# Kernel tuning notes

Measured on AMD Instinct MI355X. Metric: run time of the kernel, lower is better.

## Reference

```python
import jax, jax.numpy as jnp
import numpy as np

S_DIM, H_DIM, A_DIM, EMB, MAX_LEN = 1024, 2048, 166, 256, 20
DEC = H_DIM // 2          # decoder_hidden = 1024
VOCAB = A_DIM + 3         # 169; sos=166, eos=167, pad/ignore=168
SOS, IGNORE = A_DIM, A_DIM + 2
B = 8192


def setup_inputs() -> dict:
    key = jax.random.key(0)
    ks = jax.random.split(key, 12)
    sc = lambda fan: 1.0 / np.sqrt(fan)
    emb = jax.random.normal(ks[0], (VOCAB, EMB), jnp.float32)
    emb = emb.at[IGNORE].set(0.0)  # padding_idx=168 row is zero
    return {
        's': jax.random.normal(ks[1], (B, S_DIM), jnp.float32),
        'a_target_seq': jax.random.randint(ks[2], (B, MAX_LEN), 0, VOCAB, jnp.int32),
        'W1': jax.random.normal(ks[3], (S_DIM, H_DIM), jnp.float32) * sc(S_DIM),
        'b1': jnp.zeros((H_DIM,), jnp.float32),
        'W2': jax.random.normal(ks[4], (H_DIM, DEC), jnp.float32) * sc(H_DIM),
        'b2': jnp.zeros((DEC,), jnp.float32),
        'emb': emb,
        'Wih': jax.random.normal(ks[5], (EMB + DEC, 3 * DEC), jnp.float32) * sc(DEC),
        'Whh': jax.random.normal(ks[6], (DEC, 3 * DEC), jnp.float32) * sc(DEC),
        'bih': jnp.zeros((3 * DEC,), jnp.float32),
        'bhh': jnp.zeros((3 * DEC,), jnp.float32),
        'Wp': jax.random.normal(ks[7], (DEC, VOCAB), jnp.float32) * sc(DEC),
        'bp': jnp.zeros((VOCAB,), jnp.float32),
    }


def _gru_step(h, x, Wih, Whh, bih, bhh):
    # torch nn.GRU cell: gates ordered (r, z, n)
    gi = x @ Wih + bih                      # [B, 3H]
    gh = h @ Whh + bhh                      # [B, 3H]
    ir, iz, inn = jnp.split(gi, 3, axis=-1)
    hr, hz, hn = jnp.split(gh, 3, axis=-1)
    r = jax.nn.sigmoid(ir + hr)
    z = jax.nn.sigmoid(iz + hz)
    n = jnp.tanh(inn + r * hn)
    return (1.0 - z) * n + z * h


def reference(s, a_target_seq, W1, b1, W2, b2, emb, Wih, Whh, bih, bhh, Wp, bp):
    b = s.shape[0]
    h_s = jax.nn.relu(s @ W1 + b1) @ W2 + b2      # net(s): [B, DEC]
    h0 = h_s                                      # concatenated at every step
    # teacher forcing: input token at step t is SOS for t=0 else a_target_seq[:, t-1]
    toks = jnp.concatenate([jnp.full((b, 1), SOS, a_target_seq.dtype),
                            a_target_seq[:, :-1]], axis=1)      # [B, T]

    def step(h, tok_t):
        x = jnp.concatenate([emb[tok_t], h0], axis=-1)          # [B, EMB+DEC]
        h_new = _gru_step(h, x, Wih, Whh, bih, bhh)
        logits = h_new @ Wp + bp                                # [B, VOCAB]
        return h_new, logits

    _, logits_seq = jax.lax.scan(step, h_s, toks.T)             # [T, B, V]
    logits = jnp.transpose(logits_seq, (1, 0, 2))               # [B, T, V]

    # CrossEntropyLoss(ignore_index=IGNORE), mean over non-ignored targets
    flat_logits = logits.reshape(-1, VOCAB)
    flat_tgt = a_target_seq.reshape(-1)
    logp = jax.nn.log_softmax(flat_logits, axis=-1)
    nll = -jnp.take_along_axis(logp, flat_tgt[:, None].astype(jnp.int32), axis=-1)[:, 0]
    mask = (flat_tgt != IGNORE).astype(nll.dtype)
    loss_pred = jnp.sum(nll * mask) / jnp.maximum(jnp.sum(mask), 1.0)

    # pred_act_tsr: scatter 1.0 at per-step argmax, then drop last 3 special tokens
    eval_a = jnp.argmax(logits, axis=-1)                        # [B, T]
    pred_act_tsr = jnp.zeros((b, VOCAB), logits.dtype)
    pred_act_tsr = pred_act_tsr.at[jnp.arange(b)[:, None], eval_a].set(1.0)
    return loss_pred, pred_act_tsr[:, :-3]
```

## Files before the change

kernel.cpp:

```cpp
#include <hip/hip_runtime.h>
#include <math.h>

typedef _Float16 f16;
typedef _Float16 half8 __attribute__((ext_vector_type(8)));
typedef _Float16 half4v __attribute__((ext_vector_type(4)));
typedef float f32x4 __attribute__((ext_vector_type(4)));

#define BATCH 8192
#define SDIM  1024
#define HDIM  2048
#define DECD  1024
#define EMBD  256
#define G3    3072
#define VOCAB 169
#define VPAD  176
#define NFRAG 11
#define TLEN  20
#define SOS_TOK 166
#define IGN_TOK 168
#define OUTC  166

#define GLOAD16(gp, lp) __builtin_amdgcn_global_load_lds( \
    (const __attribute__((address_space(1))) unsigned int*)(gp), \
    (__attribute__((address_space(3))) unsigned int*)(lp), 16, 0, 0)

__device__ __forceinline__ void split2(float a, f16& h, f16& l)
{
    float hi = (fabsf(a) >= 6.103515625e-05f) ? (float)(f16)a : 0.0f;
    h = (f16)hi;
    l = (f16)((a - hi) * 2048.0f);
}

__device__ __forceinline__ float join2(f16 h, f16 l)
{
    return (float)h + (float)l * 4.8828125e-4f;
}

__device__ __forceinline__ int swz(int r, int k0)
{
    const int line = r >> 1;
    const int s = (((r & 1) << 2) | (k0 >> 3)) ^ (line & 7);
    return line * 64 + s * 8;
}

template<int MODE>
__global__ __launch_bounds__(256, 2)
void gemm16(const f16* __restrict__ Ah, const f16* __restrict__ Al,
            const f16* __restrict__ Bh, const f16* __restrict__ Bl,
            const float* __restrict__ bias, float* __restrict__ C,
            f16* __restrict__ Ch, f16* __restrict__ Cl,
            int M, int N, int K, int relu)
{
    __shared__ __align__(16) f16 lds[4][4096];

    const int nx = N >> 7;
    const int cpx = gridDim.x >> 3;
    int wg = blockIdx.x;
    wg = (wg & 7) * cpx + (wg >> 3);
    const int m0 = (wg / nx) << 7;
    const int n0 = (wg % nx) << 7;

    const int tid = threadIdx.x;
    const int w = tid >> 6;
    const int lane = tid & 63;
    const int wr = w >> 1, wc = w & 1;

    const int qq = (lane & 7) ^ (lane >> 3);
    const int row_off = ((lane >> 3) << 1) | (qq >> 2);
    const int k_off = (qq & 3) << 3;
    const f16* sb = (w == 0) ? Ah + (size_t)m0 * K
                  : (w == 1) ? Al + (size_t)m0 * K
                  : (w == 2) ? Bh + (size_t)n0 * K
                             : Bl + (size_t)n0 * K;
    sb += (size_t)row_off * K + k_off;
    f16* lb = &lds[w][0];

    int offA[4], offB[4];
    {
        const int fr = lane & 15, k0 = (lane >> 4) << 3;
#pragma unroll
        for (int t = 0; t < 4; ++t) {
            offA[t] = swz(wr * 64 + t * 16 + fr, k0);
            offB[t] = swz(wc * 64 + t * 16 + fr, k0);
        }
    }

    f32x4 acch[4][4], accl[4][4];
#pragma unroll
    for (int i = 0; i < 4; ++i)
#pragma unroll
        for (int j = 0; j < 4; ++j) { acch[i][j] = (f32x4)0.0f; accl[i][j] = (f32x4)0.0f; }

    const int nkt = K >> 5;
    const size_t K16 = (size_t)K * 16;
    for (int kt = 0; kt < nkt; ++kt) {
        const f16* s = sb + kt * 32;
#pragma unroll
        for (int i = 0; i < 8; ++i)
            GLOAD16(s + (size_t)i * K16, lb + i * 512);
        __syncthreads();

        half8 fah[4], fbh[4], fal[4], fbl[4];
#pragma unroll
        for (int t = 0; t < 4; ++t) {
            fah[t] = *(const half8*)&lds[0][offA[t]];
            fal[t] = *(const half8*)&lds[1][offA[t]];
            fbh[t] = *(const half8*)&lds[2][offB[t]];
            fbl[t] = *(const half8*)&lds[3][offB[t]];
        }
#pragma unroll
        for (int i = 0; i < 4; ++i)
#pragma unroll
            for (int j = 0; j < 4; ++j) {
                acch[i][j] = __builtin_amdgcn_mfma_f32_16x16x32_f16(fah[i], fbh[j], acch[i][j], 0, 0, 0);
                accl[i][j] = __builtin_amdgcn_mfma_f32_16x16x32_f16(fal[i], fbh[j], accl[i][j], 0, 0, 0);
                accl[i][j] = __builtin_amdgcn_mfma_f32_16x16x32_f16(fah[i], fbl[j], accl[i][j], 0, 0, 0);
            }
        __syncthreads();
    }

    const float inv2048 = 4.8828125e-4f;
    const int fr = lane & 15;
    const int fq = lane >> 4;
#pragma unroll
    for (int j = 0; j < 4; ++j) {
        const int col = n0 + wc * 64 + j * 16 + fr;
        const float bc = bias[col];
#pragma unroll
        for (int i = 0; i < 4; ++i) {
            const int row0 = m0 + wr * 64 + i * 16 + fq * 4;
            const f32x4 vh = acch[i][j], vl = accl[i][j];
#pragma unroll
            for (int r = 0; r < 4; ++r) {
                float v = vh[r] + vl[r] * inv2048 + bc;
                if (relu) v = fmaxf(v, 0.0f);
                const size_t o = (size_t)(row0 + r) * N + col;
                if constexpr (MODE & 1) C[o] = v;
                if constexpr (MODE & 2) { f16 hh, hl; split2(v, hh, hl); Ch[o] = hh; Cl[o] = hl; }
            }
        }
    }
}

#define STAGE_V2(KT) do {                                                          \
    const int ko_ = (KT) * 32 + k_off;                                             \
    if (w == 0) {                                                                  \
        const f16* sp = hch + (size_t)(m0 + row_off) * DECD + ko_;                 \
        _Pragma("unroll") for (int i_ = 0; i_ < 8; ++i_)                           \
            GLOAD16(sp + (size_t)i_ * (16 * DECD), &lds[i_ * 512]);                \
    } else if (w == 1) {                                                           \
        const f16* sp = hcl + (size_t)(m0 + row_off) * DECD + ko_;                 \
        _Pragma("unroll") for (int i_ = 0; i_ < 8; ++i_)                           \
            GLOAD16(sp + (size_t)i_ * (16 * DECD), &lds[4096 + i_ * 512]);         \
    } else if (w == 2) {                                                           \
        _Pragma("unroll") for (int g_ = 0; g_ < 3; ++g_) {                         \
            const f16* sp = whh + (size_t)(g_ * DECD + n0 + row_off) * DECD + ko_; \
            _Pragma("unroll") for (int i_ = 0; i_ < 2; ++i_)                       \
                GLOAD16(sp + (size_t)i_ * (16 * DECD),                             \
                        &lds[8192 + g_ * 1024 + i_ * 512]);                        \
        }                                                                          \
    } else {                                                                       \
        _Pragma("unroll") for (int g_ = 0; g_ < 3; ++g_) {                         \
            const f16* sp = whl + (size_t)(g_ * DECD + n0 + row_off) * DECD + ko_; \
            _Pragma("unroll") for (int i_ = 0; i_ < 2; ++i_)                       \
                GLOAD16(sp + (size_t)i_ * (16 * DECD),                             \
                        &lds[11264 + g_ * 1024 + i_ * 512]);                       \
        }                                                                          \
    }                                                                              \
} while (0)

__global__ __launch_bounds__(256, 3)
void gru_fused(const f16* __restrict__ hch, const f16* __restrict__ hcl,
               const f16* __restrict__ whh, const f16* __restrict__ whl,
               const float* __restrict__ bhh, const float* __restrict__ gx0,
               const float* __restrict__ tg, const int* __restrict__ tseq,
               int t, f16* __restrict__ hnh, f16* __restrict__ hnl)
{
    __shared__ __align__(16) f16 lds[14336];

    const int chunk = blockIdx.x & 7;
    const int q     = blockIdx.x >> 3;
    const int m0 = (q >> 2) << 7;
    const int n0 = (chunk * 4 + (q & 3)) << 5;

    const int tid = threadIdx.x, w = tid >> 6, lane = tid & 63;
    const int wr = w >> 1, wc = w & 1;

    const int qq = (lane & 7) ^ (lane >> 3);
    const int row_off = ((lane >> 3) << 1) | (qq >> 2);
    const int k_off = (qq & 3) << 3;

    const int fr = lane & 15, kq8 = (lane >> 4) << 3;
    int offA[4];
#pragma unroll
    for (int i = 0; i < 4; ++i) offA[i] = swz(wr * 64 + i * 16 + fr, kq8);
    const int offB = swz(wc * 16 + fr, kq8);

    f32x4 aH[3][4], aL[3][4];
#pragma unroll
    for (int g = 0; g < 3; ++g)
#pragma unroll
        for (int i = 0; i < 4; ++i) { aH[g][i] = (f32x4)0.0f; aL[g][i] = (f32x4)0.0f; }

    for (int kt = 0; kt < DECD / 32; ++kt) {
        STAGE_V2(kt);
        __syncthreads();

        half8 fah[4], fal[4];
#pragma unroll
        for (int i = 0; i < 4; ++i) {
            fah[i] = *(const half8*)&lds[offA[i]];
            fal[i] = *(const half8*)&lds[4096 + offA[i]];
        }
#pragma unroll
        for (int g = 0; g < 3; ++g) {
            const half8 bh = *(const half8*)&lds[8192 + g * 1024 + offB];
            const half8 bl = *(const half8*)&lds[11264 + g * 1024 + offB];
#pragma unroll
            for (int i = 0; i < 4; ++i) {
                aH[g][i] = __builtin_amdgcn_mfma_f32_16x16x32_f16(fah[i], bh, aH[g][i], 0, 0, 0);
                aL[g][i] = __builtin_amdgcn_mfma_f32_16x16x32_f16(fal[i], bh, aL[g][i], 0, 0, 0);
                aL[g][i] = __builtin_amdgcn_mfma_f32_16x16x32_f16(fah[i], bl, aL[g][i], 0, 0, 0);
            }
        }
        __syncthreads();
    }

    const float inv = 4.8828125e-4f;
    const int fq = lane >> 4;
    const int col = n0 + wc * 16 + fr;
    const float br = bhh[col];
    const float bz = bhh[DECD + col];
    const float bn = bhh[2 * DECD + col];
#pragma unroll
    for (int i = 0; i < 4; ++i) {
#pragma unroll
        for (int r = 0; r < 4; ++r) {
            const int row = m0 + wr * 64 + i * 16 + fq * 4 + r;
            const int tok = (t == 0) ? SOS_TOK : tseq[(size_t)row * TLEN + (t - 1)];
            const size_t gb = (size_t)row * G3;
            const size_t tb = (size_t)tok * G3;
            const float ghr = aH[0][i][r] + aL[0][i][r] * inv + br;
            const float ghz = aH[1][i][r] + aL[1][i][r] * inv + bz;
            const float ghn = aH[2][i][r] + aL[2][i][r] * inv + bn;
            const float gir = gx0[gb + col] + tg[tb + col];
            const float giz = gx0[gb + DECD + col] + tg[tb + DECD + col];
            const float gin = gx0[gb + 2 * DECD + col] + tg[tb + 2 * DECD + col];
            const float rr = 1.f / (1.f + expf(-(gir + ghr)));
            const float zz = 1.f / (1.f + expf(-(giz + ghz)));
            const float nn = tanhf(gin + rr * ghn);
            const size_t hidx = (size_t)row * DECD + col;
            const float hp = join2(hch[hidx], hcl[hidx]);
            const float hv = (1.f - zz) * nn + zz * hp;
            f16 a_, b_; split2(hv, a_, b_);
            hnh[hidx] = a_;
            hnl[hidx] = b_;
        }
    }
}

__global__ __launch_bounds__(256)
void transpose_split(const float* __restrict__ Wm, f16* __restrict__ th, f16* __restrict__ tl,
                     int K, int N)
{
    __shared__ float tile[32][33];
    const int n0 = blockIdx.x << 5, k0 = blockIdx.y << 5;
    const int tx = threadIdx.x & 31, ty = threadIdx.x >> 5;
#pragma unroll
    for (int j = 0; j < 32; j += 8)
        tile[ty + j][tx] = Wm[(size_t)(k0 + ty + j) * N + n0 + tx];
    __syncthreads();
#pragma unroll
    for (int j = 0; j < 32; j += 8) {
        const float a = tile[tx][ty + j];
        f16 hh, hl; split2(a, hh, hl);
        const size_t o = (size_t)(n0 + ty + j) * K + k0 + tx;
        th[o] = hh; tl[o] = hl;
    }
}

__global__ __launch_bounds__(256)
void wp_split(const float* __restrict__ Wp, f16* __restrict__ wph, f16* __restrict__ wpl)
{
    const int k = blockIdx.x * 256 + threadIdx.x;
    const int n = blockIdx.y;
    const float a = (n < VOCAB) ? Wp[(size_t)k * VOCAB + n] : 0.0f;
    f16 h, l; split2(a, h, l);
    wph[(size_t)n * DECD + k] = h;
    wpl[(size_t)n * DECD + k] = l;
}

__global__ __launch_bounds__(256)
void split_act(const float* __restrict__ x, f16* __restrict__ xh, f16* __restrict__ xl)
{
    const int i = blockIdx.x * 256 + threadIdx.x;
    const float4 v = ((const float4*)x)[i];
    half4v hh, hl;
#pragma unroll
    for (int c = 0; c < 4; ++c) { f16 a, b; split2((&v.x)[c], a, b); hh[c] = a; hl[c] = b; }
    ((half4v*)xh)[i] = hh;
    ((half4v*)xl)[i] = hl;
}

__global__ __launch_bounds__(256)
void tok_gi(const float* __restrict__ emb, const float* __restrict__ Wih,
            float* __restrict__ tg)
{
    __shared__ float es[EMBD];
    const int v = blockIdx.y;
    const int n = blockIdx.x * 256 + threadIdx.x;
    es[threadIdx.x] = emb[(size_t)v * EMBD + threadIdx.x];
    __syncthreads();
    float s = 0.f;
#pragma unroll 8
    for (int k = 0; k < EMBD; ++k)
        s = fmaf(es[k], Wih[(size_t)k * G3 + n], s);
    tg[(size_t)v * G3 + n] = s;
}

__global__ __launch_bounds__(256)
void logits_mfma(const f16* __restrict__ hh, const f16* __restrict__ hl,
                 const f16* __restrict__ wph, const f16* __restrict__ wpl,
                 const float* __restrict__ bp, const int* __restrict__ tseq,
                 int t, float* __restrict__ pred, float* __restrict__ accb)
{
    __shared__ float red[3][64][44];
    const int tid = threadIdx.x, wv = tid >> 6, lane = tid & 63;
    const int b0 = blockIdx.x << 4;
    const int fr = lane & 15, kq = lane >> 4;
    const int kb = wv << 8;

    const f16* pa_h = hh + (size_t)(b0 + fr) * DECD + kb + kq * 8;
    const f16* pa_l = hl + (size_t)(b0 + fr) * DECD + kb + kq * 8;
    const f16* pb_h = wph + (size_t)fr * DECD + kb + kq * 8;
    const f16* pb_l = wpl + (size_t)fr * DECD + kb + kq * 8;

    f32x4 acch[NFRAG], accl[NFRAG];
#pragma unroll
    for (int f = 0; f < NFRAG; ++f) { acch[f] = (f32x4)0.0f; accl[f] = (f32x4)0.0f; }

#pragma unroll 2
    for (int kt = 0; kt < 8; ++kt) {
        const int ko = kt * 32;
        const half8 a_h = *(const half8*)(pa_h + ko);
        const half8 a_l = *(const half8*)(pa_l + ko);
#pragma unroll
        for (int f = 0; f < NFRAG; ++f) {
            const half8 b_h = *(const half8*)(pb_h + (size_t)f * 16 * DECD + ko);
            const half8 b_l = *(const half8*)(pb_l + (size_t)f * 16 * DECD + ko);
            acch[f] = __builtin_amdgcn_mfma_f32_16x16x32_f16(a_h, b_h, acch[f], 0, 0, 0);
            accl[f] = __builtin_amdgcn_mfma_f32_16x16x32_f16(a_l, b_h, accl[f], 0, 0, 0);
            accl[f] = __builtin_amdgcn_mfma_f32_16x16x32_f16(a_h, b_l, accl[f], 0, 0, 0);
        }
    }

    float v[44];
#pragma unroll
    for (int f = 0; f < NFRAG; ++f)
#pragma unroll
        for (int r = 0; r < 4; ++r)
            v[f * 4 + r] = acch[f][r] + accl[f][r] * 4.8828125e-4f;

    if (wv > 0) {
#pragma unroll
        for (int idx = 0; idx < 44; ++idx) red[wv - 1][lane][idx] = v[idx];
    }
    __syncthreads();
    if (wv != 0) return;

#pragma unroll
    for (int ww = 0; ww < 3; ++ww)
#pragma unroll
        for (int idx = 0; idx < 44; ++idx) v[idx] += red[ww][lane][idx];

    float wnll = 0.f, wcnt = 0.f;
#pragma unroll
    for (int r = 0; r < 4; ++r) {
        const int b = b0 + kq * 4 + r;
        float vv[NFRAG];
        float m = -3.0e38f; int mi = 0;
#pragma unroll
        for (int f = 0; f < NFRAG; ++f) {
            const int col = f * 16 + fr;
            const float bb = (col < VOCAB) ? bp[col] : -1.0e30f;
            vv[f] = v[f * 4 + r] + bb;
            if (vv[f] > m) { m = vv[f]; mi = col; }
        }
#pragma unroll
        for (int off = 8; off >= 1; off >>= 1) {
            const float om = __shfl_xor(m, off);
            const int   oi = __shfl_xor(mi, off);
            if (om > m || (om == m && oi < mi)) { m = om; mi = oi; }
        }
        const int tgt = tseq[(size_t)b * TLEN + t];
        float se = 0.f, tl = 0.f;
#pragma unroll
        for (int f = 0; f < NFRAG; ++f) {
            se += expf(vv[f] - m);
            if ((tgt >> 4) == f && (tgt & 15) == fr) tl = vv[f];
        }
#pragma unroll
        for (int off = 8; off >= 1; off >>= 1) {
            se += __shfl_xor(se, off);
            tl += __shfl_xor(tl, off);
        }
        if (fr == 0) {
            if (mi < OUTC) pred[(size_t)b * OUTC + mi] = 1.0f;
            if (tgt != IGN_TOK) { wnll += m + logf(se) - tl; wcnt += 1.f; }
        }
    }
    wnll += __shfl_xor(wnll, 16); wnll += __shfl_xor(wnll, 32);
    wcnt += __shfl_xor(wcnt, 16); wcnt += __shfl_xor(wcnt, 32);
    if (lane == 0) {
        atomicAdd(&accb[0], wnll);
        atomicAdd(&accb[1], wcnt);
    }
}

__global__ void finalize_loss(const float* __restrict__ accb, float* __restrict__ out)
{
    out[0] = accb[0] / fmaxf(accb[1], 1.f);
}

extern "C" void kernel_launch(void* const* d_in, const int* in_sizes, int n_in,
                              void* d_out, int out_size, void* d_ws, size_t ws_size,
                              hipStream_t stream)
{
    const float* s    = (const float*)d_in[0];
    const int*   aseq = (const int*)  d_in[1];
    const float* W1   = (const float*)d_in[2];
    const float* b1   = (const float*)d_in[3];
    const float* W2   = (const float*)d_in[4];
    const float* b2   = (const float*)d_in[5];
    const float* emb  = (const float*)d_in[6];
    const float* Wih  = (const float*)d_in[7];
    const float* Whh  = (const float*)d_in[8];
    const float* bih  = (const float*)d_in[9];
    const float* bhh  = (const float*)d_in[10];
    const float* Wp   = (const float*)d_in[11];
    const float* bp   = (const float*)d_in[12];
    float* outp = (float*)d_out;
    char* W = (char*)d_ws;

    const size_t SZ_H = (size_t)BATCH * DECD * 2;
    const size_t o_gx0 = 0;
    const size_t o_hAh = o_gx0 + (size_t)BATCH * G3 * 4;
    const size_t o_hAl = o_hAh + SZ_H;
    const size_t o_hBh = o_hAl + SZ_H;
    const size_t o_hBl = o_hBh + SZ_H;
    const size_t o_tg  = o_hBl + SZ_H;
    const size_t o_whh = o_tg  + (size_t)VOCAB * G3 * 4;
    const size_t o_whl = o_whh + (size_t)DECD * G3 * 2;
    const size_t o_wph = o_whl + (size_t)DECD * G3 * 2;
    const size_t o_wpl = o_wph + (size_t)VPAD * DECD * 2;
    const size_t o_acc = o_wpl + (size_t)VPAD * DECD * 2;
    const size_t need  = o_acc + 256;
    if (ws_size < need) return;

    float* gx0  = (float*)(W + o_gx0);
    f16*   hAh  = (f16*)(W + o_hAh);
    f16*   hAl  = (f16*)(W + o_hAl);
    f16*   hBh  = (f16*)(W + o_hBh);
    f16*   hBl  = (f16*)(W + o_hBl);
    float* tg   = (float*)(W + o_tg);
    f16*   whh  = (f16*)(W + o_whh);
    f16*   whl  = (f16*)(W + o_whl);
    f16*   wph  = (f16*)(W + o_wph);
    f16*   wpl  = (f16*)(W + o_wpl);
    float* accb = (float*)(W + o_acc);

    f16* h1h = (f16*)(W + o_gx0);
    f16* h1l = (f16*)(W + o_gx0 + (size_t)BATCH * HDIM * 2);
    f16* w1h = (f16*)(W + o_gx0 + (size_t)BATCH * HDIM * 4);
    f16* w1l = (f16*)(W + o_gx0 + (size_t)BATCH * HDIM * 4 + (size_t)SDIM * HDIM * 2);
    f16* w2h = w1h;
    f16* w2l = (f16*)(W + o_gx0 + (size_t)BATCH * HDIM * 4 + (size_t)HDIM * DECD * 2);
    f16* sh  = (f16*)(W + o_hBh);
    f16* sl  = (f16*)(W + o_hBh + (size_t)BATCH * SDIM * 2);
    f16* wih = whh;
    f16* wil = whl;

    hipMemsetAsync(d_out, 0, (size_t)out_size * sizeof(float), stream);
    hipMemsetAsync(accb, 0, 2 * sizeof(float), stream);

    split_act<<<dim3(BATCH * SDIM / 4 / 256), 256, 0, stream>>>(s, sh, sl);
    transpose_split<<<dim3(HDIM/32, SDIM/32), 256, 0, stream>>>(W1, w1h, w1l, SDIM, HDIM);
    tok_gi<<<dim3(G3/256, VOCAB), 256, 0, stream>>>(emb, Wih, tg);
    wp_split<<<dim3(DECD/256, VPAD), 256, 0, stream>>>(Wp, wph, wpl);

    gemm16<2><<<dim3((BATCH/128)*(HDIM/128)), 256, 0, stream>>>(
        sh, sl, w1h, w1l, b1, nullptr, h1h, h1l, BATCH, HDIM, SDIM, 1);

    transpose_split<<<dim3(DECD/32, HDIM/32), 256, 0, stream>>>(W2, w2h, w2l, HDIM, DECD);
    gemm16<2><<<dim3((BATCH/128)*(DECD/128)), 256, 0, stream>>>(
        h1h, h1l, w2h, w2l, b2, nullptr, hAh, hAl, BATCH, DECD, HDIM, 0);

    transpose_split<<<dim3(G3/32, DECD/32), 256, 0, stream>>>(Wih + (size_t)EMBD * G3, wih, wil, DECD, G3);
    gemm16<1><<<dim3((BATCH/128)*(G3/128)), 256, 0, stream>>>(
        hAh, hAl, wih, wil, bih, gx0, nullptr, nullptr, BATCH, G3, DECD, 0);

    transpose_split<<<dim3(G3/32, DECD/32), 256, 0, stream>>>(Whh, whh, whl, DECD, G3);

    f16 *ch = hAh, *cl = hAl, *nh = hBh, *nl = hBl;
    for (int t = 0; t < TLEN; ++t) {
        gru_fused<<<dim3((BATCH/128)*(DECD/32)), 256, 0, stream>>>(
            ch, cl, whh, whl, bhh, gx0, tg, aseq, t, nh, nl);
        logits_mfma<<<dim3(BATCH/16), 256, 0, stream>>>(
            nh, nl, wph, wpl, bp, aseq, t, outp + 1, accb);
        f16* tmp;
        tmp = ch; ch = nh; nh = tmp;
        tmp = cl; cl = nl; nl = tmp;
    }
    finalize_loss<<<1, 1, 0, stream>>>(accb, outp);
}
```

Measured before the change: 5.722 ms.

## Fuse GRU step and previous-step logits into one launch with block specialization

Merges the per-step GRU kernel and the logits/loss kernel into a single launch. Extra blocks compute logits for the previous step's hidden state while the GRU blocks compute the next step, so the two phases overlap and the number of launches drops. The logits work is split by vocab fragments across waves instead of by K, with a small LDS reduction, and Wp padding grows to 192 columns. In exchange the launch carries heterogeneous blocks that share one register and launch-bounds budget, and an extra launch is needed after the loop to finish the final step's logits.

Measured after the change: 5.762 ms. About the same (+0.7%).

```diff
diff --git a/kernel.cpp b/kernel.cpp
--- a/kernel.cpp
+++ b/kernel.cpp
@@ -13,12 +13,14 @@
 #define EMBD  256
 #define G3    3072
 #define VOCAB 169
-#define VPAD  176
+#define VPADX 192
 #define NFRAG 11
 #define TLEN  20
 #define SOS_TOK 166
 #define IGN_TOK 168
 #define OUTC  166
+#define NGRU_BLK 2048
+#define NLOG_BLK 512
 
 #define GLOAD16(gp, lp) __builtin_amdgcn_global_load_lds( \
     (const __attribute__((address_space(1))) unsigned int*)(gp), \
@@ -170,91 +172,203 @@
 } while (0)
 
 __global__ __launch_bounds__(256, 3)
-void gru_fused(const f16* __restrict__ hch, const f16* __restrict__ hcl,
-               const f16* __restrict__ whh, const f16* __restrict__ whl,
-               const float* __restrict__ bhh, const float* __restrict__ gx0,
-               const float* __restrict__ tg, const int* __restrict__ tseq,
-               int t, f16* __restrict__ hnh, f16* __restrict__ hnl)
+void step_fused(const f16* __restrict__ hch, const f16* __restrict__ hcl,
+                const f16* __restrict__ whh, const f16* __restrict__ whl,
+                const float* __restrict__ bhh, const float* __restrict__ gx0,
+                const float* __restrict__ tg, const int* __restrict__ tseq,
+                int t, f16* __restrict__ hnh, f16* __restrict__ hnl,
+                const f16* __restrict__ wph, const f16* __restrict__ wpl,
+                const float* __restrict__ bp, int tlog,
+                float* __restrict__ pred, float* __restrict__ accb,
+                int ngru)
 {
     __shared__ __align__(16) f16 lds[14336];
 
-    const int chunk = blockIdx.x & 7;
-    const int q     = blockIdx.x >> 3;
-    const int m0 = (q >> 2) << 7;
-    const int n0 = (chunk * 4 + (q & 3)) << 5;
-
-    const int tid = threadIdx.x, w = tid >> 6, lane = tid & 63;
-    const int wr = w >> 1, wc = w & 1;
-
-    const int qq = (lane & 7) ^ (lane >> 3);
-    const int row_off = ((lane >> 3) << 1) | (qq >> 2);
-    const int k_off = (qq & 3) << 3;
-
-    const int fr = lane & 15, kq8 = (lane >> 4) << 3;
-    int offA[4];
-#pragma unroll
-    for (int i = 0; i < 4; ++i) offA[i] = swz(wr * 64 + i * 16 + fr, kq8);
-    const int offB = swz(wc * 16 + fr, kq8);
-
-    f32x4 aH[3][4], aL[3][4];
-#pragma unroll
-    for (int g = 0; g < 3; ++g)
-#pragma unroll
-        for (int i = 0; i < 4; ++i) { aH[g][i] = (f32x4)0.0f; aL[g][i] = (f32x4)0.0f; }
-
-    for (int kt = 0; kt < DECD / 32; ++kt) {
-        STAGE_V2(kt);
+    if ((int)blockIdx.x < ngru) {
+        const int chunk = blockIdx.x & 7;
+        const int q     = blockIdx.x >> 3;
+        const int m0 = (q >> 2) << 7;
+        const int n0 = (chunk * 4 + (q & 3)) << 5;
+
+        const int tid = threadIdx.x, w = tid >> 6, lane = tid & 63;
+        const int wr = w >> 1, wc = w & 1;
+
+        const int qq = (lane & 7) ^ (lane >> 3);
+        const int row_off = ((lane >> 3) << 1) | (qq >> 2);
+        const int k_off = (qq & 3) << 3;
+
+        const int fr = lane & 15, kq8 = (lane >> 4) << 3;
+        int offA[4];
+#pragma unroll
+        for (int i = 0; i < 4; ++i) offA[i] = swz(wr * 64 + i * 16 + fr, kq8);
+        const int offB = swz(wc * 16 + fr, kq8);
+
+        f32x4 aH[3][4], aL[3][4];
+#pragma unroll
+        for (int g = 0; g < 3; ++g)
+#pragma unroll
+            for (int i = 0; i < 4; ++i) { aH[g][i] = (f32x4)0.0f; aL[g][i] = (f32x4)0.0f; }
+
+        for (int kt = 0; kt < DECD / 32; ++kt) {
+            STAGE_V2(kt);
+            __syncthreads();
+
+            half8 fah[4], fal[4];
+#pragma unroll
+            for (int i = 0; i < 4; ++i) {
+                fah[i] = *(const half8*)&lds[offA[i]];
+                fal[i] = *(const half8*)&lds[4096 + offA[i]];
+            }
+#pragma unroll
+            for (int g = 0; g < 3; ++g) {
+                const half8 bh = *(const half8*)&lds[8192 + g * 1024 + offB];
+                const half8 bl = *(const half8*)&lds[11264 + g * 1024 + offB];
+#pragma unroll
+                for (int i = 0; i < 4; ++i) {
+                    aH[g][i] = __builtin_amdgcn_mfma_f32_16x16x32_f16(fah[i], bh, aH[g][i], 0, 0, 0);
+                    aL[g][i] = __builtin_amdgcn_mfma_f32_16x16x32_f16(fal[i], bh, aL[g][i], 0, 0, 0);
+                    aL[g][i] = __builtin_amdgcn_mfma_f32_16x16x32_f16(fah[i], bl, aL[g][i], 0, 0, 0);
+                }
+            }
+            __syncthreads();
+        }
+
+        const float inv = 4.8828125e-4f;
+        const int fq = lane >> 4;
+        const int col = n0 + wc * 16 + fr;
+        const float br = bhh[col];
+        const float bz = bhh[DECD + col];
+        const float bn = bhh[2 * DECD + col];
+#pragma unroll
+        for (int i = 0; i < 4; ++i) {
+#pragma unroll
+            for (int r = 0; r < 4; ++r) {
+                const int row = m0 + wr * 64 + i * 16 + fq * 4 + r;
+                const int tok = (t == 0) ? SOS_TOK : tseq[(size_t)row * TLEN + (t - 1)];
+                const size_t gb = (size_t)row * G3;
+                const size_t tb = (size_t)tok * G3;
+                const float ghr = aH[0][i][r] + aL[0][i][r] * inv + br;
+                const float ghz = aH[1][i][r] + aL[1][i][r] * inv + bz;
+                const float ghn = aH[2][i][r] + aL[2][i][r] * inv + bn;
+                const float gir = gx0[gb + col] + tg[tb + col];
+                const float giz = gx0[gb + DECD + col] + tg[tb + DECD + col];
+                const float gin = gx0[gb + 2 * DECD + col] + tg[tb + 2 * DECD + col];
+                const float rr = 1.f / (1.f + expf(-(gir + ghr)));
+                const float zz = 1.f / (1.f + expf(-(giz + ghz)));
+                const float nn = tanhf(gin + rr * ghn);
+                const size_t hidx = (size_t)row * DECD + col;
+                const float hp = join2(hch[hidx], hcl[hidx]);
+                const float hv = (1.f - zz) * nn + zz * hp;
+                f16 a_, b_; split2(hv, a_, b_);
+                hnh[hidx] = a_;
+                hnl[hidx] = b_;
+            }
+        }
+    } else {
+        float* red = (float*)&lds[0];
+        const int tid = threadIdx.x, wv = tid >> 6, lane = tid & 63;
+        const int lb = blockIdx.x - ngru;
+        const int b0 = lb << 4;
+        const int fr = lane & 15, kq = lane >> 4;
+        const int fb0 = wv * 3;
+
+        const f16* pa_h = hch + (size_t)(b0 + fr) * DECD + kq * 8;
+        const f16* pa_l = hcl + (size_t)(b0 + fr) * DECD + kq * 8;
+        const f16* pb_h = wph + (size_t)(fb0 * 16 + fr) * DECD + kq * 8;
+        const f16* pb_l = wpl + (size_t)(fb0 * 16 + fr) * DECD + kq * 8;
+
+        f32x4 acch[3], accl[3];
+#pragma unroll
+        for (int f = 0; f < 3; ++f) { acch[f] = (f32x4)0.0f; accl[f] = (f32x4)0.0f; }
+
+#pragma unroll 2
+        for (int kt = 0; kt < 32; ++kt) {
+            const int ko = kt * 32;
+            const half8 a_h = *(const half8*)(pa_h + ko);
+            const half8 a_l = *(const half8*)(pa_l + ko);
+#pragma unroll
+            for (int f = 0; f < 3; ++f) {
+                const half8 b_h = *(const half8*)(pb_h + (size_t)f * 16 * DECD + ko);
+                const half8 b_l = *(const half8*)(pb_l + (size_t)f * 16 * DECD + ko);
+                acch[f] = __builtin_amdgcn_mfma_f32_16x16x32_f16(a_h, b_h, acch[f], 0, 0, 0);
+                accl[f] = __builtin_amdgcn_mfma_f32_16x16x32_f16(a_l, b_h, accl[f], 0, 0, 0);
+                accl[f] = __builtin_amdgcn_mfma_f32_16x16x32_f16(a_h, b_l, accl[f], 0, 0, 0);
+            }
+        }
+
+        const float inv = 4.8828125e-4f;
+#pragma unroll
+        for (int r = 0; r < 4; ++r) {
+            float vv[3];
+            float m = -3.0e38f; int mi = 0;
+#pragma unroll
+            for (int f = 0; f < 3; ++f) {
+                const int col = (fb0 + f) * 16 + fr;
+                const float bb = (col < VOCAB) ? bp[col] : -1.0e30f;
+                vv[f] = acch[f][r] + accl[f][r] * inv + bb;
+                if (vv[f] > m) { m = vv[f]; mi = col; }
+            }
+#pragma unroll
+            for (int off = 8; off >= 1; off >>= 1) {
+                const float om = __shfl_xor(m, off);
+                const int   oi = __shfl_xor(mi, off);
+                if (om > m || (om == m && oi < mi)) { m = om; mi = oi; }
+            }
+            const int b = b0 + kq * 4 + r;
+            const int tgt = tseq[(size_t)b * TLEN + tlog];
+            float se = 0.f, tl = 0.f;
+#pragma unroll
+            for (int f = 0; f < 3; ++f) {
+                se += expf(vv[f] - m);
+                const int col = (fb0 + f) * 16 + fr;
+                if (col == tgt) tl = vv[f];
+            }
+#pragma unroll
+            for (int off = 8; off >= 1; off >>= 1) {
+                se += __shfl_xor(se, off);
+                tl += __shfl_xor(tl, off);
+            }
+            if (fr == 0) {
+                const int row = kq * 4 + r;
+                red[(wv * 16 + row) * 4 + 0] = m;
+                red[(wv * 16 + row) * 4 + 1] = (float)mi;
+                red[(wv * 16 + row) * 4 + 2] = se;
+                red[(wv * 16 + row) * 4 + 3] = tl;
+            }
+        }
         __syncthreads();
 
-        half8 fah[4], fal[4];
-#pragma unroll
-        for (int i = 0; i < 4; ++i) {
-            fah[i] = *(const half8*)&lds[offA[i]];
-            fal[i] = *(const half8*)&lds[4096 + offA[i]];
-        }
-#pragma unroll
-        for (int g = 0; g < 3; ++g) {
-            const half8 bh = *(const half8*)&lds[8192 + g * 1024 + offB];
-            const half8 bl = *(const half8*)&lds[11264 + g * 1024 + offB];
-#pragma unroll
-            for (int i = 0; i < 4; ++i) {
-                aH[g][i] = __builtin_amdgcn_mfma_f32_16x16x32_f16(fah[i], bh, aH[g][i], 0, 0, 0);
-                aL[g][i] = __builtin_amdgcn_mfma_f32_16x16x32_f16(fal[i], bh, aL[g][i], 0, 0, 0);
-                aL[g][i] = __builtin_amdgcn_mfma_f32_16x16x32_f16(fah[i], bl, aL[g][i], 0, 0, 0);
-            }
-        }
-        __syncthreads();
-    }
-
-    const float inv = 4.8828125e-4f;
-    const int fq = lane >> 4;
-    const int col = n0 + wc * 16 + fr;
-    const float br = bhh[col];
-    const float bz = bhh[DECD + col];
-    const float bn = bhh[2 * DECD + col];
-#pragma unroll
-    for (int i = 0; i < 4; ++i) {
-#pragma unroll
-        for (int r = 0; r < 4; ++r) {
-            const int row = m0 + wr * 64 + i * 16 + fq * 4 + r;
-            const int tok = (t == 0) ? SOS_TOK : tseq[(size_t)row * TLEN + (t - 1)];
-            const size_t gb = (size_t)row * G3;
-            const size_t tb = (size_t)tok * G3;
-            const float ghr = aH[0][i][r] + aL[0][i][r] * inv + br;
-            const float ghz = aH[1][i][r] + aL[1][i][r] * inv + bz;
-            const float ghn = aH[2][i][r] + aL[2][i][r] * inv + bn;
-            const float gir = gx0[gb + col] + tg[tb + col];
-            const float giz = gx0[gb + DECD + col] + tg[tb + DECD + col];
-            const float gin = gx0[gb + 2 * DECD + col] + tg[tb + 2 * DECD + col];
-            const float rr = 1.f / (1.f + expf(-(gir + ghr)));
-            const float zz = 1.f / (1.f + expf(-(giz + ghz)));
-            const float nn = tanhf(gin + rr * ghn);
-            const size_t hidx = (size_t)row * DECD + col;
-            const float hp = join2(hch[hidx], hcl[hidx]);
-            const float hv = (1.f - zz) * nn + zz * hp;
-            f16 a_, b_; split2(hv, a_, b_);
-            hnh[hidx] = a_;
-            hnl[hidx] = b_;
+        float wnll = 0.f, wcnt = 0.f;
+        if (wv == 0 && lane < 16) {
+            const int row = lane;
+            float M = red[row * 4 + 0];
+            int  MI = (int)red[row * 4 + 1];
+#pragma unroll
+            for (int wq = 1; wq < 4; ++wq) {
+                const float mw = red[(wq * 16 + row) * 4 + 0];
+                if (mw > M) { M = mw; MI = (int)red[(wq * 16 + row) * 4 + 1]; }
+            }
+            float se = 0.f, tl = 0.f;
+#pragma unroll
+            for (int wq = 0; wq < 4; ++wq) {
+                se += red[(wq * 16 + row) * 4 + 2] * expf(red[(wq * 16 + row) * 4 + 0] - M);
+                tl += red[(wq * 16 + row) * 4 + 3];
+            }
+            const int b = b0 + row;
+            if (MI < OUTC) pred[(size_t)b * OUTC + MI] = 1.0f;
+            const int tgt = tseq[(size_t)b * TLEN + tlog];
+            if (tgt != IGN_TOK) { wnll = M + logf(se) - tl; wcnt = 1.f; }
+        }
+        if (wv == 0) {
+#pragma unroll
+            for (int off = 32; off >= 1; off >>= 1) {
+                wnll += __shfl_xor(wnll, off);
+                wcnt += __shfl_xor(wcnt, off);
+            }
+            if (lane == 0) {
+                atomicAdd(&accb[0], wnll);
+                atomicAdd(&accb[1], wcnt);
+            }
         }
     }
 }
@@ -316,105 +430,6 @@
     for (int k = 0; k < EMBD; ++k)
         s = fmaf(es[k], Wih[(size_t)k * G3 + n], s);
     tg[(size_t)v * G3 + n] = s;
-}
-
-__global__ __launch_bounds__(256)
-void logits_mfma(const f16* __restrict__ hh, const f16* __restrict__ hl,
-                 const f16* __restrict__ wph, const f16* __restrict__ wpl,
-                 const float* __restrict__ bp, const int* __restrict__ tseq,
-                 int t, float* __restrict__ pred, float* __restrict__ accb)
-{
-    __shared__ float red[3][64][44];
-    const int tid = threadIdx.x, wv = tid >> 6, lane = tid & 63;
-    const int b0 = blockIdx.x << 4;
-    const int fr = lane & 15, kq = lane >> 4;
-    const int kb = wv << 8;
-
-    const f16* pa_h = hh + (size_t)(b0 + fr) * DECD + kb + kq * 8;
-    const f16* pa_l = hl + (size_t)(b0 + fr) * DECD + kb + kq * 8;
-    const f16* pb_h = wph + (size_t)fr * DECD + kb + kq * 8;
-    const f16* pb_l = wpl + (size_t)fr * DECD + kb + kq * 8;
-
-    f32x4 acch[NFRAG], accl[NFRAG];
-#pragma unroll
-    for (int f = 0; f < NFRAG; ++f) { acch[f] = (f32x4)0.0f; accl[f] = (f32x4)0.0f; }
-
-#pragma unroll 2
-    for (int kt = 0; kt < 8; ++kt) {
-        const int ko = kt * 32;
-        const half8 a_h = *(const half8*)(pa_h + ko);
-        const half8 a_l = *(const half8*)(pa_l + ko);
-#pragma unroll
-        for (int f = 0; f < NFRAG; ++f) {
-            const half8 b_h = *(const half8*)(pb_h + (size_t)f * 16 * DECD + ko);
-            const half8 b_l = *(const half8*)(pb_l + (size_t)f * 16 * DECD + ko);
-            acch[f] = __builtin_amdgcn_mfma_f32_16x16x32_f16(a_h, b_h, acch[f], 0, 0, 0);
-            accl[f] = __builtin_amdgcn_mfma_f32_16x16x32_f16(a_l, b_h, accl[f], 0, 0, 0);
-            accl[f] = __builtin_amdgcn_mfma_f32_16x16x32_f16(a_h, b_l, accl[f], 0, 0, 0);
-        }
-    }
-
-    float v[44];
-#pragma unroll
-    for (int f = 0; f < NFRAG; ++f)
-#pragma unroll
-        for (int r = 0; r < 4; ++r)
-            v[f * 4 + r] = acch[f][r] + accl[f][r] * 4.8828125e-4f;
-
-    if (wv > 0) {
-#pragma unroll
-        for (int idx = 0; idx < 44; ++idx) red[wv - 1][lane][idx] = v[idx];
-    }
-    __syncthreads();
-    if (wv != 0) return;
-
-#pragma unroll
-    for (int ww = 0; ww < 3; ++ww)
-#pragma unroll
-        for (int idx = 0; idx < 44; ++idx) v[idx] += red[ww][lane][idx];
-
-    float wnll = 0.f, wcnt = 0.f;
-#pragma unroll
-    for (int r = 0; r < 4; ++r) {
-        const int b = b0 + kq * 4 + r;
-        float vv[NFRAG];
-        float m = -3.0e38f; int mi = 0;
-#pragma unroll
-        for (int f = 0; f < NFRAG; ++f) {
-            const int col = f * 16 + fr;
-            const float bb = (col < VOCAB) ? bp[col] : -1.0e30f;
-            vv[f] = v[f * 4 + r] + bb;
-            if (vv[f] > m) { m = vv[f]; mi = col; }
-        }
-#pragma unroll
-        for (int off = 8; off >= 1; off >>= 1) {
-            const float om = __shfl_xor(m, off);
-            const int   oi = __shfl_xor(mi, off);
-            if (om > m || (om == m && oi < mi)) { m = om; mi = oi; }
-        }
-        const int tgt = tseq[(size_t)b * TLEN + t];
-        float se = 0.f, tl = 0.f;
-#pragma unroll
-        for (int f = 0; f < NFRAG; ++f) {
-            se += expf(vv[f] - m);
-            if ((tgt >> 4) == f && (tgt & 15) == fr) tl = vv[f];
-        }
-#pragma unroll
-        for (int off = 8; off >= 1; off >>= 1) {
-            se += __shfl_xor(se, off);
-            tl += __shfl_xor(tl, off);
-        }
-        if (fr == 0) {
-            if (mi < OUTC) pred[(size_t)b * OUTC + mi] = 1.0f;
-            if (tgt != IGN_TOK) { wnll += m + logf(se) - tl; wcnt += 1.f; }
-        }
-    }
-    wnll += __shfl_xor(wnll, 16); wnll += __shfl_xor(wnll, 32);
-    wcnt += __shfl_xor(wcnt, 16); wcnt += __shfl_xor(wcnt, 32);
-    if (lane == 0) {
-        atomicAdd(&accb[0], wnll);
-        atomicAdd(&accb[1], wcnt);
-    }
 }
 
 __global__ void finalize_loss(const float* __restrict__ accb, float* __restrict__ out)
@@ -452,8 +467,8 @@
     const size_t o_whh = o_tg  + (size_t)VOCAB * G3 * 4;
     const size_t o_whl = o_whh + (size_t)DECD * G3 * 2;
     const size_t o_wph = o_whl + (size_t)DECD * G3 * 2;
-    const size_t o_wpl = o_wph + (size_t)VPAD * DECD * 2;
-    const size_t o_acc = o_wpl + (size_t)VPAD * DECD * 2;
+    const size_t o_wpl = o_wph + (size_t)VPADX * DECD * 2;
+    const size_t o_acc = o_wpl + (size_t)VPADX * DECD * 2;
     const size_t need  = o_acc + 256;
     if (ws_size < need) return;
 
@@ -486,7 +501,7 @@
     split_act<<<dim3(BATCH * SDIM / 4 / 256), 256, 0, stream>>>(s, sh, sl);
     transpose_split<<<dim3(HDIM/32, SDIM/32), 256, 0, stream>>>(W1, w1h, w1l, SDIM, HDIM);
     tok_gi<<<dim3(G3/256, VOCAB), 256, 0, stream>>>(emb, Wih, tg);
-    wp_split<<<dim3(DECD/256, VPAD), 256, 0, stream>>>(Wp, wph, wpl);
+    wp_split<<<dim3(DECD/256, VPADX), 256, 0, stream>>>(Wp, wph, wpl);
 
     gemm16<2><<<dim3((BATCH/128)*(HDIM/128)), 256, 0, stream>>>(
         sh, sl, w1h, w1l, b1, nullptr, h1h, h1l, BATCH, HDIM, SDIM, 1);
@@ -502,14 +517,21 @@
     transpose_split<<<dim3(G3/32, DECD/32), 256, 0, stream>>>(Whh, whh, whl, DECD, G3);
 
     f16 *ch = hAh, *cl = hAl, *nh = hBh, *nl = hBl;
-    for (int t = 0; t < TLEN; ++t) {
-        gru_fused<<<dim3((BATCH/128)*(DECD/32)), 256, 0, stream>>>(
-            ch, cl, whh, whl, bhh, gx0, tg, aseq, t, nh, nl);
-        logits_mfma<<<dim3(BATCH/16), 256, 0, stream>>>(
-            nh, nl, wph, wpl, bp, aseq, t, outp + 1, accb);
-        f16* tmp;
-        tmp = ch; ch = nh; nh = tmp;
+    step_fused<<<dim3(NGRU_BLK), 256, 0, stream>>>(
+        ch, cl, whh, whl, bhh, gx0, tg, aseq, 0, nh, nl,
+        wph, wpl, bp, 0, outp + 1, accb, NGRU_BLK);
+    { f16* tmp = ch; ch = nh; nh = tmp; tmp = cl; cl = nl; nl = tmp; }
+
+    for (int t = 1; t < TLEN; ++t) {
+        step_fused<<<dim3(NGRU_BLK + NLOG_BLK), 256, 0, stream>>>(
+            ch, cl, whh, whl, bhh, gx0, tg, aseq, t, nh, nl,
+            wph, wpl, bp, t - 1, outp + 1, accb, NGRU_BLK);
+        f16* tmp = ch; ch = nh; nh = tmp;
         tmp = cl; cl = nl; nl = tmp;
     }
+    step_fused<<<dim3(NLOG_BLK), 256, 0, stream>>>(
+        ch, cl, whh, whl, bhh, gx0, tg, aseq, 0, nh, nl,
+        wph, wpl, bp, TLEN - 1, outp + 1, accb, 0);
+
     finalize_loss<<<1, 1, 0, stream>>>(accb, outp);
 }
```

## Double-buffer LDS staging in fused GRU recurrent GEMM to overlap loads with MFMA

Applied to the files above, without the earlier changes.

Splits the LDS tile buffer into two sets so the async global-to-LDS loads for the next K tile are issued while MFMAs run on the current one. This halves the barriers per K step and hides global load latency behind compute. LDS per block doubles to about 57 KB, and launch bounds drop from 3 to 2 blocks per SM, so occupancy falls.

After: 6.373 ms. 1.11x slower.

```diff
diff --git a/kernel.cpp b/kernel.cpp
--- a/kernel.cpp
+++ b/kernel.cpp
@@ -142,41 +142,59 @@
     }
 }
 
-#define STAGE_V2(KT) do {                                                          \
+#define STAGE_DB(SET, KT) do {                                                     \
     const int ko_ = (KT) * 32 + k_off;                                             \
+    f16* lb_ = &lds[SET][0];                                                       \
     if (w == 0) {                                                                  \
         const f16* sp = hch + (size_t)(m0 + row_off) * DECD + ko_;                 \
         _Pragma("unroll") for (int i_ = 0; i_ < 8; ++i_)                           \
-            GLOAD16(sp + (size_t)i_ * (16 * DECD), &lds[i_ * 512]);                \
+            GLOAD16(sp + (size_t)i_ * (16 * DECD), lb_ + i_ * 512);                \
     } else if (w == 1) {                                                           \
         const f16* sp = hcl + (size_t)(m0 + row_off) * DECD + ko_;                 \
         _Pragma("unroll") for (int i_ = 0; i_ < 8; ++i_)                           \
-            GLOAD16(sp + (size_t)i_ * (16 * DECD), &lds[4096 + i_ * 512]);         \
+            GLOAD16(sp + (size_t)i_ * (16 * DECD), lb_ + 4096 + i_ * 512);         \
     } else if (w == 2) {                                                           \
         _Pragma("unroll") for (int g_ = 0; g_ < 3; ++g_) {                         \
             const f16* sp = whh + (size_t)(g_ * DECD + n0 + row_off) * DECD + ko_; \
             _Pragma("unroll") for (int i_ = 0; i_ < 2; ++i_)                       \
                 GLOAD16(sp + (size_t)i_ * (16 * DECD),                             \
-                        &lds[8192 + g_ * 1024 + i_ * 512]);                        \
+                        lb_ + 8192 + g_ * 1024 + i_ * 512);                        \
         }                                                                          \
     } else {                                                                       \
         _Pragma("unroll") for (int g_ = 0; g_ < 3; ++g_) {                         \
             const f16* sp = whl + (size_t)(g_ * DECD + n0 + row_off) * DECD + ko_; \
             _Pragma("unroll") for (int i_ = 0; i_ < 2; ++i_)                       \
                 GLOAD16(sp + (size_t)i_ * (16 * DECD),                             \
-                        &lds[11264 + g_ * 1024 + i_ * 512]);                       \
+                        lb_ + 11264 + g_ * 1024 + i_ * 512);                       \
         }                                                                          \
     }                                                                              \
 } while (0)
 
-__global__ __launch_bounds__(256, 3)
+#define COMPUTE_DB(SET) do {                                                       \
+    half8 fah[4], fal[4];                                                          \
+    _Pragma("unroll") for (int i_ = 0; i_ < 4; ++i_) {                             \
+        fah[i_] = *(const half8*)&lds[SET][offA[i_]];                              \
+        fal[i_] = *(const half8*)&lds[SET][4096 + offA[i_]];                       \
+    }                                                                              \
+    _Pragma("unroll") for (int g_ = 0; g_ < 3; ++g_) {                             \
+        const half8 bh = *(const half8*)&lds[SET][8192 + g_ * 1024 + offB];        \
+        const half8 bl = *(const half8*)&lds[SET][11264 + g_ * 1024 + offB];       \
+        _Pragma("unroll") for (int i_ = 0; i_ < 4; ++i_) {                         \
+            aH[g_][i_] = __builtin_amdgcn_mfma_f32_16x16x32_f16(fah[i_], bh, aH[g_][i_], 0, 0, 0); \
+            aL[g_][i_] = __builtin_amdgcn_mfma_f32_16x16x32_f16(fal[i_], bh, aL[g_][i_], 0, 0, 0); \
+            aL[g_][i_] = __builtin_amdgcn_mfma_f32_16x16x32_f16(fah[i_], bl, aL[g_][i_], 0, 0, 0); \
+        }                                                                          \
+    }                                                                              \
+} while (0)
+
+__global__ __launch_bounds__(256, 2)
 void gru_fused(const f16* __restrict__ hch, const f16* __restrict__ hcl,
                const f16* __restrict__ whh, const f16* __restrict__ whl,
                const float* __restrict__ bhh, const float* __restrict__ gx0,
                const float* __restrict__ tg, const int* __restrict__ tseq,
                int t, f16* __restrict__ hnh, f16* __restrict__ hnl)
 {
-    __shared__ __align__(16) f16 lds[14336];
+    __shared__ __align__(16) f16 lds[2][14336];
 
     const int chunk = blockIdx.x & 7;
     const int q     = blockIdx.x >> 3;
@@ -202,27 +220,15 @@
 #pragma unroll
         for (int i = 0; i < 4; ++i) { aH[g][i] = (f32x4)0.0f; aL[g][i] = (f32x4)0.0f; }
 
-    for (int kt = 0; kt < DECD / 32; ++kt) {
-        STAGE_V2(kt);
+    STAGE_DB(0, 0);
+    __syncthreads();
+
+    for (int kt = 0; kt < DECD / 32; kt += 2) {
+        STAGE_DB(1, kt + 1);
+        COMPUTE_DB(0);
         __syncthreads();
-
-        half8 fah[4], fal[4];
-#pragma unroll
-        for (int i = 0; i < 4; ++i) {
-            fah[i] = *(const half8*)&lds[offA[i]];
-            fal[i] = *(const half8*)&lds[4096 + offA[i]];
-        }
-#pragma unroll
-        for (int g = 0; g < 3; ++g) {
-            const half8 bh = *(const half8*)&lds[8192 + g * 1024 + offB];
-            const half8 bl = *(const half8*)&lds[11264 + g * 1024 + offB];
-#pragma unroll
-            for (int i = 0; i < 4; ++i) {
-                aH[g][i] = __builtin_amdgcn_mfma_f32_16x16x32_f16(fah[i], bh, aH[g][i], 0, 0, 0);
-                aL[g][i] = __builtin_amdgcn_mfma_f32_16x16x32_f16(fal[i], bh, aL[g][i], 0, 0, 0);
-                aL[g][i] = __builtin_amdgcn_mfma_f32_16x16x32_f16(fah[i], bl, aL[g][i], 0, 0, 0);
-            }
-        }
+        if (kt + 2 < DECD / 32) STAGE_DB(0, kt + 2);
+        COMPUTE_DB(1);
         __syncthreads();
     }
 
```
